# Performance work log

Hardware: AMD Instinct MI355X
Metric: run time of the kernel (lower is better)

Reference implementation:

```python
import jax, jax.numpy as jnp
import numpy as np

GROUP = 16
IN_F = 4096
OUT_F = 4096
FP4_LEVELS = jnp.array([0.0, 0.5, 1.0, 1.5, 2.0, 3.0, 4.0, 6.0], dtype=jnp.float32)
# midpoints between consecutive fp4 magnitudes (round-to-nearest boundaries)
FP4_MIDS = jnp.array([0.25, 0.75, 1.25, 1.75, 2.5, 3.5, 5.0], dtype=jnp.float32)

def _e4m3_pos_table():
    bits = np.arange(127)  # positive e4m3 values, excluding NaN pattern 127
    e = bits >> 3
    m = bits & 7
    vals = np.where(e == 0, (m / 8.0) * 2.0 ** -6, (1.0 + m / 8.0) * 2.0 ** (e - 7.0))
    return jnp.asarray(vals, dtype=jnp.float32)

E4M3_POS = _e4m3_pos_table()

def e4m3_decode(bits):
    # bits: int array holding e4m3 bit patterns
    s = (bits >> 7) & 1
    e = ((bits >> 3) & 15).astype(jnp.float32)
    m = (bits & 7).astype(jnp.float32)
    mag = jnp.where(e == 0, (m / 8.0) * (2.0 ** -6), (1.0 + m / 8.0) * jnp.exp2(e - 7.0))
    return jnp.where(s == 1, -mag, mag).astype(jnp.float32)

def e4m3_round(x):
    # round non-negative x to nearest representable e4m3 value (returns float)
    x = jnp.clip(x, 0.0, 448.0)
    idx = jnp.clip(jnp.searchsorted(E4M3_POS, x), 1, 126)
    lo = E4M3_POS[idx - 1]
    hi = E4M3_POS[idx]
    return jnp.where(x - lo <= hi - x, lo, hi)

def fp4_decode(code):
    mag = FP4_LEVELS[code & 7]
    return jnp.where(code >= 8, -mag, mag)

def fp4_round(y):
    # round to nearest E2M1 value; clamp magnitude to 6
    a = jnp.minimum(jnp.abs(y), 6.0)
    idx = jnp.searchsorted(FP4_MIDS, a, side='right')
    return jnp.sign(y) * FP4_LEVELS[idx]

def nvfp4_quant_dequant(x2d, input_scale):
    # activation quantization: per-16 block e4m3 scale on top of per-tensor scale
    M, K = x2d.shape
    xb = x2d.reshape(M, K // GROUP, GROUP)
    amax = jnp.max(jnp.abs(xb), axis=-1, keepdims=True)
    bscale = e4m3_round(amax / (6.0 * input_scale))  # decoded e4m3 block scale
    eff = bscale * input_scale
    safe = jnp.where(eff > 0, eff, 1.0)
    q = fp4_round(xb / safe)
    return (q * eff).reshape(M, K)

def dequant_weight(weight, weight_scale, weight_scale_2):
    lo = weight & 15
    hi = (weight >> 4) & 15
    codes = jnp.stack([lo, hi], axis=-1).reshape(OUT_F, IN_F)  # [out, in]
    w = fp4_decode(codes)
    bs = e4m3_decode(weight_scale)  # [out, in//16]
    scale = jnp.repeat(bs, GROUP, axis=-1) * weight_scale_2  # [out, in]
    return w * scale

def setup_inputs() -> dict:
    key = jax.random.key(0)
    k1, k2, k3 = jax.random.split(key, 3)
    x = jax.random.normal(k1, (4, 2048, IN_F), dtype=jnp.float32)
    weight = jax.random.randint(k2, (OUT_F, IN_F // 2), 0, 256, dtype=jnp.int32)
    # e4m3 bit patterns with exponent in [4, 9], sign 0 -> scales ~[0.125, 3.75]
    weight_scale = jax.random.randint(k3, (OUT_F, IN_F // GROUP), 32, 80, dtype=jnp.int32)
    weight_scale_2 = jnp.array([0.02], dtype=jnp.float32)
    input_scale = jnp.array([0.01], dtype=jnp.float32)
    return {"x": x, "weight": weight, "weight_scale": weight_scale,
            "weight_scale_2": weight_scale_2, "input_scale": input_scale}

def reference(x, weight, weight_scale, weight_scale_2, input_scale):
    in_shape = x.shape
    x2d = x.reshape(-1, in_shape[-1])
    xd = nvfp4_quant_dequant(x2d, input_scale)           # quantize+dequant activations
    w = dequant_weight(weight, weight_scale, weight_scale_2)  # dequant fp4 weights
    out = jnp.einsum('mk,nk->mn', xd, w)                 # F.linear
    return out.reshape(*in_shape[:-1], OUT_F)
```

## Files before the change

kernel.cpp:

```cpp
#include <hip/hip_runtime.h>
#include <stdint.h>

#define IN_F  4096
#define OUT_F 4096
#define MROWS 8192

typedef __bf16 bf16x8 __attribute__((ext_vector_type(8)));
typedef float  f32x4  __attribute__((ext_vector_type(4)));


__device__ __forceinline__ float e4m3_round_dev(float x) {
    x = fminf(x, 448.0f);
    float lo, hi;
    if (x < 0.015625f) {
        lo = floorf(x * 512.0f) * 0.001953125f;
        hi = lo + 0.001953125f;
    } else {
        unsigned u = __float_as_uint(x);
        int E = (int)((u >> 23) & 0xFF) - 127;
        float step  = __uint_as_float((unsigned)(E + 124) << 23);
        float istep = __uint_as_float((unsigned)(130 - E) << 23);
        lo = floorf(x * istep) * step;
        hi = lo + step;
    }
    return (x - lo <= hi - x) ? lo : hi;
}

__device__ __forceinline__ float e4m3_decode_dev(int bits) {
    int e = (bits >> 3) & 15;
    int m = bits & 7;
    float mag;
    if (e == 0) mag = (float)m * 0.001953125f;
    else        mag = (1.0f + (float)m * 0.125f) * __uint_as_float((unsigned)(e + 120) << 23);
    return (bits & 0x80) ? -mag : mag;
}

__device__ __forceinline__ float fp4_round_dev(float y) {
    float a = fminf(fabsf(y), 6.0f);
    float v;
    if (a < 1.75f) {
        if (a < 0.75f) v = (a < 0.25f) ? 0.0f : 0.5f;
        else           v = (a < 1.25f) ? 1.0f : 1.5f;
    } else {
        if (a < 3.5f)  v = (a < 2.5f) ? 2.0f : 3.0f;
        else           v = (a < 5.0f) ? 4.0f : 6.0f;
    }
    return copysignf(v, y);
}

__device__ __forceinline__ float fp4_decode_dev(int c) {
    int e = (c >> 1) & 3, m = c & 1;
    float mag = (e == 0) ? 0.5f * (float)m
                         : (1.0f + 0.5f * (float)m) * __uint_as_float((unsigned)(e + 126) << 23);
    return (c & 8) ? -mag : mag;
}

__device__ __forceinline__ unsigned pack_bf16x2(float a, float b) {
    return (__float_as_uint(a) >> 16) | ((__float_as_uint(b) >> 16) << 16);
}

__global__ __launch_bounds__(256) void quant_act_kernel(
    const float* __restrict__ x, const float* __restrict__ in_scale,
    unsigned short* __restrict__ Aq)
{
    int t = blockIdx.x * 256 + threadIdx.x;
    const float isc = in_scale[0];
    float4 v = ((const float4*)x)[t];

    float a = fmaxf(fmaxf(fabsf(v.x), fabsf(v.y)), fmaxf(fabsf(v.z), fabsf(v.w)));
    a = fmaxf(a, __shfl_xor(a, 1));
    a = fmaxf(a, __shfl_xor(a, 2));

    float bscale = e4m3_round_dev(a / (6.0f * isc));
    float eff = bscale * isc;
    float safe = (eff > 0.0f) ? eff : 1.0f;
    float inv = 1.0f / safe;

    unsigned o0 = pack_bf16x2(fp4_round_dev(v.x * inv) * bscale,
                              fp4_round_dev(v.y * inv) * bscale);
    unsigned o1 = pack_bf16x2(fp4_round_dev(v.z * inv) * bscale,
                              fp4_round_dev(v.w * inv) * bscale);
    ((uint2*)Aq)[t] = make_uint2(o0, o1);
}

__global__ __launch_bounds__(256) void dequant_w_kernel(
    const int* __restrict__ wq, const int* __restrict__ wsb,
    unsigned short* __restrict__ Wd)
{
    int t = blockIdx.x * 256 + threadIdx.x;
    float scale = e4m3_decode_dev(wsb[t >> 1]);
    int4 b = ((const int4*)wq)[t];
    int bytes[4] = { b.x, b.y, b.z, b.w };
    unsigned out[4];
    #pragma unroll
    for (int i = 0; i < 4; i++) {
        int by = bytes[i];
        float v0 = fp4_decode_dev(by & 15) * scale;
        float v1 = fp4_decode_dev((by >> 4) & 15) * scale;
        out[i] = pack_bf16x2(v0, v1);
    }
    ((uint4*)Wd)[t] = make_uint4(out[0], out[1], out[2], out[3]);
}


__device__ __forceinline__ void gload16(const void* g, void* l) {
    __builtin_amdgcn_global_load_lds((__attribute__((address_space(1))) void*)g,
                                     (__attribute__((address_space(3))) void*)l,
                                     16, 0, 0);
}

#define BARRIER() __builtin_amdgcn_s_barrier()
#define FENCE() asm volatile("" ::: "memory")
#define WAIT_VM(n) asm volatile("s_waitcnt vmcnt(" #n ")" ::: "memory")

#define STAGE(q, par, dt) do {                                                 \
    const unsigned short* g_ = ((q) >= 2 ? gA[(q)-2] : gB[(q)]) + (dt) * 64;   \
    char* l_ = ldsb + ((q) >= 2 ? (par)*32768 + ((q)-2)*16384                  \
                                : 65536 + (par)*32768 + (q)*16384) + ldst0;    \
    gload16(g_, l_);                                                           \
    gload16(g_ + CH2, l_ + 8192);                                              \
} while (0)

#define LOADA(par, qm) do {                                                    \
    const char* pa_ = ldsb + (par)*32768 + aRd + (qm)*8192;                    \
    _Pragma("unroll") for (int m_ = 0; m_ < 4; ++m_) {                         \
        af[m_][0] = *(const bf16x8*)(pa_ + m_*2048 + sw0);                     \
        af[m_][1] = *(const bf16x8*)(pa_ + m_*2048 + (sw0 ^ 64));              \
    }                                                                          \
} while (0)

#define LOADB01(par) do {                                                      \
    const char* pb_ = ldsb + (par)*32768 + bRd;                                \
    _Pragma("unroll") for (int n_ = 0; n_ < 2; ++n_) {                         \
        bf[n_][0] = *(const bf16x8*)(pb_ + n_*2048 + sw0);                     \
        bf[n_][1] = *(const bf16x8*)(pb_ + n_*2048 + (sw0 ^ 64));              \
    }                                                                          \
} while (0)

#define LOADB23(par) do {                                                      \
    const char* pb_ = ldsb + (par)*32768 + bRd;                                \
    _Pragma("unroll") for (int n_ = 2; n_ < 4; ++n_) {                         \
        bf[n_][0] = *(const bf16x8*)(pb_ + n_*2048 + sw0);                     \
        bf[n_][1] = *(const bf16x8*)(pb_ + n_*2048 + (sw0 ^ 64));              \
    }                                                                          \
} while (0)

#define MFMAQ(qm, qn) do {                                                     \
    __builtin_amdgcn_s_setprio(1);                                             \
    _Pragma("unroll") for (int m_ = 0; m_ < 4; ++m_)                           \
      _Pragma("unroll") for (int n_ = 0; n_ < 2; ++n_)                         \
        _Pragma("unroll") for (int kh_ = 0; kh_ < 2; ++kh_)                    \
          acc[(qm)*4 + m_][(qn)*2 + n_] =                                      \
            __builtin_amdgcn_mfma_f32_16x16x32_bf16(                           \
              af[m_][kh_], bf[(qn)*2 + n_][kh_],                               \
              acc[(qm)*4 + m_][(qn)*2 + n_], 0, 0, 0);                         \
    __builtin_amdgcn_s_setprio(0);                                             \
} while (0)

#define KTILE(par, DT, SN, SB2, VMODE) do {                                    \
                                                                      \
    LOADB01(par); LOADA(par, 0);                                               \
    if (SN) { STAGE(2, (par) ^ 1, (DT) + 1); STAGE(1, (par) ^ 1, (DT) + 1); }  \
    BARRIER(); FENCE();                                                        \
    MFMAQ(0, 0);                                                               \
                                                                      \
    LOADB23(par);                                                              \
    if (SN) STAGE(3, (par) ^ 1, (DT) + 1);                                     \
    BARRIER(); FENCE();                                                        \
    MFMAQ(0, 1);                                                               \
                                                                      \
    LOADA(par, 1);                                                             \
    BARRIER(); FENCE();                                                        \
    MFMAQ(1, 0);                                                               \
                                                                      \
    if (SB2) STAGE(0, (par), (DT) + 2);                                        \
    if ((VMODE) == 2) { WAIT_VM(2); } else if ((VMODE) == 0) { WAIT_VM(0); }   \
    BARRIER(); FENCE();                                                        \
    MFMAQ(1, 1);                                                               \
} while (0)

__global__ __launch_bounds__(512, 2) void gemm256(
    const unsigned short* __restrict__ A, const unsigned short* __restrict__ B,
    float* __restrict__ C, const float* __restrict__ isc,
    const float* __restrict__ ws2)
{
    extern __shared__ __align__(16) char lds[];
    char* const ldsb = lds;

    const int tid  = threadIdx.x;
    const int lane = tid & 63;
    const int w    = tid >> 6;
    const int wm   = w >> 2;
    const int wn   = w & 3;

    int bid = blockIdx.x;
    int swz = (bid & 7) * 64 + (bid >> 3);
    const int bm = swz >> 4;
    const int bn = swz & 15;

    const int row0 = tid >> 3;
    const int kc0  = (tid & 7) ^ (row0 & 7);
    const size_t CH2 = (size_t)64 * IN_F;
    const unsigned short* gA[2];
    const unsigned short* gB[2];
    gA[0] = A + (size_t)(bm * 256 +   0 + row0) * IN_F + kc0 * 8;
    gA[1] = A + (size_t)(bm * 256 + 128 + row0) * IN_F + kc0 * 8;
    gB[0] = B + (size_t)(bn * 256 +   0 + row0) * IN_F + kc0 * 8;
    gB[1] = B + (size_t)(bn * 256 + 128 + row0) * IN_F + kc0 * 8;
    const int ldst0 = tid * 16;

    const int l16 = lane & 15, quad = lane >> 4, x7 = l16 & 7;
    const int sw0 = ((quad ^ x7) << 4);
    const int aRd = wm * 16384 + l16 * 128;
    const int bRd = 65536 + (wn >> 1) * 16384 + (wn & 1) * 8192 + l16 * 128;

    f32x4 acc[8][4];
    #pragma unroll
    for (int i = 0; i < 8; ++i)
        #pragma unroll
        for (int j = 0; j < 4; ++j)
            acc[i][j] = (f32x4){0.f, 0.f, 0.f, 0.f};
    bf16x8 af[4][2];
    bf16x8 bf[4][2];

    STAGE(0, 0, 0); STAGE(2, 0, 0); STAGE(1, 0, 0); STAGE(3, 0, 0);
    STAGE(0, 1, 1);
    WAIT_VM(2);
    BARRIER(); FENCE();

    #pragma unroll 1
    for (int tt = 0; tt < 62; tt += 2) {
        KTILE(0, 0, 1, 1, 2);
        KTILE(1, 1, 1, 1, 2);
        gA[0] += 128; gA[1] += 128; gB[0] += 128; gB[1] += 128;
    }
    KTILE(0, 0, 1, 0, 0);
    KTILE(1, 1, 0, 0, -1);

    const float s = isc[0] * ws2[0];
    #pragma unroll
    for (int M = 0; M < 8; ++M) {
        int r0 = bm * 256 + wm * 128 + M * 16 + quad * 4;
        #pragma unroll
        for (int n = 0; n < 4; ++n) {
            int col = bn * 256 + wn * 64 + n * 16 + l16;
            float* cp = C + (size_t)r0 * OUT_F + col;
            #pragma unroll
            for (int r = 0; r < 4; ++r)
                cp[(size_t)r * OUT_F] = acc[M][n][r] * s;
        }
    }
}

extern "C" void kernel_launch(void* const* d_in, const int* in_sizes, int n_in,
                              void* d_out, int out_size, void* d_ws, size_t ws_size,
                              hipStream_t stream) {
    const float* x   = (const float*)d_in[0];
    const int*   wq  = (const int*)d_in[1];
    const int*   wsb = (const int*)d_in[2];
    const float* ws2 = (const float*)d_in[3];
    const float* isc = (const float*)d_in[4];
    float* out = (float*)d_out;

    unsigned short* Aq = (unsigned short*)d_ws;
    unsigned short* Wd = (unsigned short*)d_ws + (size_t)MROWS * IN_F;

    static int attr_done = 0;
    if (!attr_done) {
        hipFuncSetAttribute(reinterpret_cast<const void*>(gemm256),
                            hipFuncAttributeMaxDynamicSharedMemorySize, 131072);
        attr_done = 1;
    }

    quant_act_kernel<<<32768, 256, 0, stream>>>(x, isc, Aq);
    dequant_w_kernel<<<8192, 256, 0, stream>>>(wq, wsb, Wd);
    gemm256<<<512, 512, 131072, stream>>>(Aq, Wd, out, isc, ws2);

    (void)in_sizes; (void)n_in; (void)out_size; (void)ws_size;
}
```

Baseline: 452.7 us.

## Switch GEMM to 128x256 tiles with K-step 32 and 256-thread blocks

Replaces the 256x256 block tile (512 threads, 128KB LDS, K-step 64 with multi-stage prefetch) with a 128x256 tile using 256 threads, 48KB LDS and K-step 32 double buffering. Each wave now covers the full 128-row M by 64 columns, and the LDS swizzle is adapted to 64-byte rows. The aim is higher occupancy and a simpler pipeline, at the cost of lower operand reuse per block, more barriers per unit of work, and a full vmcnt(0) wait each half-tile.

```diff
diff --git a/kernel.cpp b/kernel.cpp
--- a/kernel.cpp
+++ b/kernel.cpp
@@ -113,73 +113,58 @@
 #define FENCE() asm volatile("" ::: "memory")
 #define WAIT_VM(n) asm volatile("s_waitcnt vmcnt(" #n ")" ::: "memory")
 
-#define STAGE(q, par, dt) do {                                                 \
-    const unsigned short* g_ = ((q) >= 2 ? gA[(q)-2] : gB[(q)]) + (dt) * 64;   \
-    char* l_ = ldsb + ((q) >= 2 ? (par)*32768 + ((q)-2)*16384                  \
-                                : 65536 + (par)*32768 + (q)*16384) + ldst0;    \
-    gload16(g_, l_);                                                           \
-    gload16(g_ + CH2, l_ + 8192);                                              \
-} while (0)
-
-#define LOADA(par, qm) do {                                                    \
-    const char* pa_ = ldsb + (par)*32768 + aRd + (qm)*8192;                    \
-    _Pragma("unroll") for (int m_ = 0; m_ < 4; ++m_) {                         \
-        af[m_][0] = *(const bf16x8*)(pa_ + m_*2048 + sw0);                     \
-        af[m_][1] = *(const bf16x8*)(pa_ + m_*2048 + (sw0 ^ 64));              \
-    }                                                                          \
-} while (0)
-
-#define LOADB01(par) do {                                                      \
-    const char* pb_ = ldsb + (par)*32768 + bRd;                                \
-    _Pragma("unroll") for (int n_ = 0; n_ < 2; ++n_) {                         \
-        bf[n_][0] = *(const bf16x8*)(pb_ + n_*2048 + sw0);                     \
-        bf[n_][1] = *(const bf16x8*)(pb_ + n_*2048 + (sw0 ^ 64));              \
-    }                                                                          \
-} while (0)
-
-#define LOADB23(par) do {                                                      \
-    const char* pb_ = ldsb + (par)*32768 + bRd;                                \
-    _Pragma("unroll") for (int n_ = 2; n_ < 4; ++n_) {                         \
-        bf[n_][0] = *(const bf16x8*)(pb_ + n_*2048 + sw0);                     \
-        bf[n_][1] = *(const bf16x8*)(pb_ + n_*2048 + (sw0 ^ 64));              \
-    }                                                                          \
-} while (0)
-
-#define MFMAQ(qm, qn) do {                                                     \
+#define STAGE_A(par, dt) do {                                                  \
+    const unsigned short* g_ = gA0 + (dt) * 32;                                \
+    char* l_ = ldsb + (par) * 8192 + tid * 16;                                 \
+    gload16(g_,              l_);                                              \
+    gload16(g_ + 64 * IN_F,  l_ + 4096);                                       \
+} while (0)
+
+#define STAGE_B(par, dt) do {                                                  \
+    const unsigned short* g_ = gB0 + (dt) * 32;                                \
+    char* l_ = ldsb + 16384 + (par) * 16384 + tid * 16;                        \
+    gload16(g_,               l_);                                             \
+    gload16(g_ + 64  * IN_F,  l_ + 4096);                                      \
+    gload16(g_ + 128 * IN_F,  l_ + 8192);                                      \
+    gload16(g_ + 192 * IN_F,  l_ + 12288);                                     \
+} while (0)
+
+#define LOADAF(par, qm) do {                                                   \
+    const char* pa_ = ldsb + (par) * 8192 + (qm) * 4096 + aBase;               \
+    _Pragma("unroll") for (int m_ = 0; m_ < 4; ++m_)                           \
+        af[m_] = *(const bf16x8*)(pa_ + m_ * 1024);                            \
+} while (0)
+
+#define LOADBF(par) do {                                                       \
+    const char* pb_ = ldsb + 16384 + (par) * 16384 + bBase;                    \
+    _Pragma("unroll") for (int n_ = 0; n_ < 4; ++n_)                           \
+        bf[n_] = *(const bf16x8*)(pb_ + n_ * 1024);                            \
+} while (0)
+
+#define MFMAQ(qm) do {                                                         \
     __builtin_amdgcn_s_setprio(1);                                             \
     _Pragma("unroll") for (int m_ = 0; m_ < 4; ++m_)                           \
-      _Pragma("unroll") for (int n_ = 0; n_ < 2; ++n_)                         \
-        _Pragma("unroll") for (int kh_ = 0; kh_ < 2; ++kh_)                    \
-          acc[(qm)*4 + m_][(qn)*2 + n_] =                                      \
+      _Pragma("unroll") for (int n_ = 0; n_ < 4; ++n_)                         \
+          acc[(qm)*4 + m_][n_] =                                               \
             __builtin_amdgcn_mfma_f32_16x16x32_bf16(                           \
-              af[m_][kh_], bf[(qn)*2 + n_][kh_],                               \
-              acc[(qm)*4 + m_][(qn)*2 + n_], 0, 0, 0);                         \
+              af[m_], bf[n_], acc[(qm)*4 + m_][n_], 0, 0, 0);                  \
     __builtin_amdgcn_s_setprio(0);                                             \
 } while (0)
 
-#define KTILE(par, DT, SN, SB2, VMODE) do {                                    \
+#define KTILE(par, DT, SN, VM) do {                                            \
                                                                       \
-    LOADB01(par); LOADA(par, 0);                                               \
-    if (SN) { STAGE(2, (par) ^ 1, (DT) + 1); STAGE(1, (par) ^ 1, (DT) + 1); }  \
+    LOADAF(par, 0); LOADBF(par);                                               \
+    if (SN) { STAGE_B((par) ^ 1, (DT) + 1); STAGE_A((par) ^ 1, (DT) + 1); }    \
     BARRIER(); FENCE();                                                        \
-    MFMAQ(0, 0);                                                               \
+    MFMAQ(0);                                                                  \
                                                                       \
-    LOADB23(par);                                                              \
-    if (SN) STAGE(3, (par) ^ 1, (DT) + 1);                                     \
+    LOADAF(par, 1);                                                            \
+    if (VM) { WAIT_VM(0); }                                                    \
     BARRIER(); FENCE();                                                        \
-    MFMAQ(0, 1);                                                               \
-                                                                      \
-    LOADA(par, 1);                                                             \
-    BARRIER(); FENCE();                                                        \
-    MFMAQ(1, 0);                                                               \
-                                                                      \
-    if (SB2) STAGE(0, (par), (DT) + 2);                                        \
-    if ((VMODE) == 2) { WAIT_VM(2); } else if ((VMODE) == 0) { WAIT_VM(0); }   \
-    BARRIER(); FENCE();                                                        \
-    MFMAQ(1, 1);                                                               \
-} while (0)
-
-__global__ __launch_bounds__(512, 2) void gemm256(
+    MFMAQ(1);                                                                  \
+} while (0)
+
+__global__ __launch_bounds__(256, 2) void gemm128x256(
     const unsigned short* __restrict__ A, const unsigned short* __restrict__ B,
     float* __restrict__ C, const float* __restrict__ isc,
     const float* __restrict__ ws2)
@@ -189,30 +174,22 @@
 
     const int tid  = threadIdx.x;
     const int lane = tid & 63;
-    const int w    = tid >> 6;
-    const int wm   = w >> 2;
-    const int wn   = w & 3;
+    const int wn   = tid >> 6;
 
     int bid = blockIdx.x;
-    int swz = (bid & 7) * 64 + (bid >> 3);
-    const int bm = swz >> 4;
-    const int bn = swz & 15;
-
-    const int row0 = tid >> 3;
-    const int kc0  = (tid & 7) ^ (row0 & 7);
-    const size_t CH2 = (size_t)64 * IN_F;
-    const unsigned short* gA[2];
-    const unsigned short* gB[2];
-    gA[0] = A + (size_t)(bm * 256 +   0 + row0) * IN_F + kc0 * 8;
-    gA[1] = A + (size_t)(bm * 256 + 128 + row0) * IN_F + kc0 * 8;
-    gB[0] = B + (size_t)(bn * 256 +   0 + row0) * IN_F + kc0 * 8;
-    gB[1] = B + (size_t)(bn * 256 + 128 + row0) * IN_F + kc0 * 8;
-    const int ldst0 = tid * 16;
-
-    const int l16 = lane & 15, quad = lane >> 4, x7 = l16 & 7;
-    const int sw0 = ((quad ^ x7) << 4);
-    const int aRd = wm * 16384 + l16 * 128;
-    const int bRd = 65536 + (wn >> 1) * 16384 + (wn & 1) * 8192 + l16 * 128;
+    int swz = (bid & 7) * 128 + (bid >> 3);
+    const int bm = swz & 63;
+    const int bn = swz >> 6;
+
+    const int rowS = tid >> 2;
+    const int kc0  = (tid & 3) ^ ((tid >> 3) & 3);
+    const unsigned short* gA0 = A + (size_t)(bm * 128 + rowS) * IN_F + kc0 * 8;
+    const unsigned short* gB0 = B + (size_t)(bn * 256 + rowS) * IN_F + kc0 * 8;
+
+    const int l16 = lane & 15, quad = lane >> 4;
+    const int swz16 = ((quad ^ ((l16 >> 1) & 3)) << 4);
+    const int aBase = l16 * 64 + swz16;
+    const int bBase = wn * 4096 + l16 * 64 + swz16;
 
     f32x4 acc[8][4];
     #pragma unroll
@@ -220,27 +197,26 @@
         #pragma unroll
         for (int j = 0; j < 4; ++j)
             acc[i][j] = (f32x4){0.f, 0.f, 0.f, 0.f};
-    bf16x8 af[4][2];
-    bf16x8 bf[4][2];
-
-    STAGE(0, 0, 0); STAGE(2, 0, 0); STAGE(1, 0, 0); STAGE(3, 0, 0);
-    STAGE(0, 1, 1);
-    WAIT_VM(2);
+    bf16x8 af[4];
+    bf16x8 bf[4];
+
+    STAGE_B(0, 0); STAGE_A(0, 0);
+    WAIT_VM(0);
     BARRIER(); FENCE();
 
     #pragma unroll 1
-    for (int tt = 0; tt < 62; tt += 2) {
-        KTILE(0, 0, 1, 1, 2);
-        KTILE(1, 1, 1, 1, 2);
-        gA[0] += 128; gA[1] += 128; gB[0] += 128; gB[1] += 128;
-    }
-    KTILE(0, 0, 1, 0, 0);
-    KTILE(1, 1, 0, 0, -1);
+    for (int tt = 0; tt < 126; tt += 2) {
+        KTILE(0, 0, 1, 1);
+        KTILE(1, 1, 1, 1);
+        gA0 += 64; gB0 += 64;
+    }
+    KTILE(0, 0, 1, 1);
+    KTILE(1, 1, 0, 0);
 
     const float s = isc[0] * ws2[0];
     #pragma unroll
     for (int M = 0; M < 8; ++M) {
-        int r0 = bm * 256 + wm * 128 + M * 16 + quad * 4;
+        int r0 = bm * 128 + M * 16 + quad * 4;
         #pragma unroll
         for (int n = 0; n < 4; ++n) {
             int col = bn * 256 + wn * 64 + n * 16 + l16;
@@ -267,14 +243,14 @@
 
     static int attr_done = 0;
     if (!attr_done) {
-        hipFuncSetAttribute(reinterpret_cast<const void*>(gemm256),
-                            hipFuncAttributeMaxDynamicSharedMemorySize, 131072);
+        hipFuncSetAttribute(reinterpret_cast<const void*>(gemm128x256),
+                            hipFuncAttributeMaxDynamicSharedMemorySize, 49152);
         attr_done = 1;
     }
 
     quant_act_kernel<<<32768, 256, 0, stream>>>(x, isc, Aq);
     dequant_w_kernel<<<8192, 256, 0, stream>>>(wq, wsb, Wd);
-    gemm256<<<512, 512, 131072, stream>>>(Aq, Wd, out, isc, ws2);
+    gemm128x256<<<1024, 256, 49152, stream>>>(Aq, Wd, out, isc, ws2);
 
     (void)in_sizes; (void)n_in; (void)out_size; (void)ws_size;
 }
```

After: 505.0 us. +11.5%, slower.
